# Optimization experiments

Measured on AMD Instinct MI355X. Metric: run time of the kernel, lower is better.

Reference implementation:

```python
import jax, jax.numpy as jnp
import numpy as np

N, L, LEADS = 512, 640, 3
COND_DIM, NUM_K, DIM_K = 1, 100, 5
FLAT = 256 * 79  # 20224, from conv stack trace


def _leaky(x):
    return jnp.where(x >= 0, x, 0.2 * x)


def _sn(w, u):
    # PyTorch spectral_norm: one power iteration (u, v detached), sigma = u^T W v
    wm = w.reshape(w.shape[0], -1)
    v = wm.T @ u
    v = v / (jnp.linalg.norm(v) + 1e-12)
    u2 = wm @ v
    u2 = u2 / (jnp.linalg.norm(u2) + 1e-12)
    u2 = jax.lax.stop_gradient(u2)
    v = jax.lax.stop_gradient(v)
    sigma = u2 @ (wm @ v)
    return w / sigma


def _conv1d(x, w, b, stride, pad):
    y = jax.lax.conv_general_dilated(
        x, w, window_strides=(stride,), padding=[(pad, pad)],
        dimension_numbers=('NCH', 'OIH', 'NCH'))
    return y + b[None, :, None]


def setup_inputs() -> dict:
    key = jax.random.key(0)
    ks = jax.random.split(key, 16)
    g = lambda k, shp, s: (jax.random.normal(k, shp, dtype=jnp.float32) * s)
    inp = {
        'ecg': jax.random.normal(ks[0], (N, L, LEADS), dtype=jnp.float32),
        'condition': jax.random.randint(ks[1], (N, 1), 0, 4),
        'w1': g(ks[2], (64, LEADS, 5), 0.2), 'b1': jnp.zeros((64,), jnp.float32),
        'u1': jax.random.normal(ks[3], (64,), dtype=jnp.float32),
        'w2': g(ks[4], (128, 64, 7), 0.05), 'b2': jnp.zeros((128,), jnp.float32),
        'u2': jax.random.normal(ks[5], (128,), dtype=jnp.float32),
        'w3': g(ks[6], (256, 128, 9), 0.03), 'b3': jnp.zeros((256,), jnp.float32),
        'u3': jax.random.normal(ks[7], (256,), dtype=jnp.float32),
        'emb': g(ks[8], (4, COND_DIM), 1.0),
        'cond_w': g(ks[9], (50, COND_DIM), 0.5), 'cond_b': jnp.zeros((50,), jnp.float32),
        'mb_w': g(ks[10], (FLAT, NUM_K * DIM_K), 0.01),
        'fc_w': g(ks[11], (1, FLAT + NUM_K + 50), 0.01), 'fc_b': jnp.zeros((1,), jnp.float32),
    }
    return inp


def reference(ecg, condition, w1, b1, u1, w2, b2, u2, w3, b3, u3,
              emb, cond_w, cond_b, mb_w, fc_w, fc_b):
    # condition embedding -> Linear(cond_dim, 50)
    cemb = emb[condition[:, 0]]                       # [N, cond_dim]
    cond = cemb @ cond_w.T + cond_b                   # [N, 50]

    x = ecg.transpose(0, 2, 1)                        # [N, 3, 640]
    x = _leaky(_conv1d(x, _sn(w1, u1), b1, 2, 4))     # [N, 64, 322]
    x = _leaky(_conv1d(x, _sn(w2, u2), b2, 2, 3))     # [N, 128, 161]
    x = _leaky(_conv1d(x, _sn(w3, u3), b3, 2, 2))     # [N, 256, 79]
    flat = x.reshape(x.shape[0], -1)                  # [N, 20224]

    # minibatch discrimination
    act = (flat @ mb_w).reshape(-1, NUM_K, DIM_K)     # [N, K, D]
    l1 = jnp.abs(act[:, None] - act[None, :]).sum(-1)  # [N, N, K]
    feats = jnp.exp(-l1).sum(axis=1)                  # [N, K]

    out = jnp.concatenate([flat, feats, cond], axis=1)
    return out @ fc_w.T + fc_b                        # [N, 1]
```

## Files before the change

kernel.cpp:

```cpp
#include <hip/hip_runtime.h>
#include <math.h>

#define NB 512
#define LIN 640
#define NLEADS 3
#define L1O 322
#define L2O 161
#define L3O 79
#define C1N 64
#define C2N 128
#define C3N 256
#define FLATSZ 20224
#define NUMK 100
#define DIMK 5
#define SPLITK 16

typedef __attribute__((ext_vector_type(8))) short short8;
typedef __attribute__((ext_vector_type(4))) float f32x4;

__device__ __forceinline__ unsigned short f2bf(float x){
  unsigned u = __builtin_bit_cast(unsigned, x);
  unsigned r = u + 0x7FFFu + ((u >> 16) & 1u);
  return (unsigned short)(r >> 16);
}
__device__ __forceinline__ float bf2f(unsigned short x){
  unsigned u = ((unsigned)x) << 16;
  return __builtin_bit_cast(float, u);
}

__device__ __forceinline__ float block_reduce_sum(float val, float* red){
#pragma unroll
  for(int off=32; off>0; off>>=1) val += __shfl_down(val, off, 64);
  int lane = threadIdx.x & 63;
  int wv = threadIdx.x >> 6;
  if(lane==0) red[wv] = val;
  __syncthreads();
  int nw = blockDim.x >> 6;
  float r = red[0];
  for(int i=1;i<nw;i++) r += red[i];
  __syncthreads();
  return r;
}

__global__ __launch_bounds__(256)
void sn_pass1(const float* __restrict__ w1, const float* __restrict__ u1,
              const float* __restrict__ w2, const float* __restrict__ u2,
              const float* __restrict__ w3, const float* __restrict__ u3,
              float* __restrict__ v_all, float* __restrict__ ss){
  __shared__ float red[4];
  int b = blockIdx.x, tid = threadIdx.x;
  const float* w; const float* u; int O, C, off, c, widx;
  if(b==0){ w=w1; u=u1; O=64;  C=15;   off=0;   c=tid;            widx=0; }
  else if(b<3){ w=w2; u=u2; O=128; C=448; off=16;  c=(b-1)*256+tid; widx=1; }
  else { w=w3; u=u3; O=256; C=1152; off=464; c=(b-3)*256+tid;      widx=2; }
  float vv = 0.f;
  if(c < C){
    for(int o=0;o<O;o+=4){
      vv += w[(o+0)*C+c]*u[o+0] + w[(o+1)*C+c]*u[o+1]
          + w[(o+2)*C+c]*u[o+2] + w[(o+3)*C+c]*u[o+3];
    }
    v_all[off + c] = vv;
  }
  float ps = (c < C) ? vv*vv : 0.f;
  float tot = block_reduce_sum(ps, red);
  if(tid==0) atomicAdd(&ss[widx], tot);
}

__global__ __launch_bounds__(256)
void sn_pass2(const float* __restrict__ w1, const float* __restrict__ w2,
              const float* __restrict__ w3, const float* __restrict__ v_all,
              float* __restrict__ Sun){
  int b = blockIdx.x, tid = threadIdx.x;
  int lane = tid & 63, wv = tid >> 6;
  const float* w; int C, off, o, widx;
  if(b < 16){ w=w1; C=15;   off=0;   o=b*4+wv;      widx=0; }
  else if(b < 48){ w=w2; C=448; off=16;  o=(b-16)*4+wv; widx=1; }
  else { w=w3; C=1152; off=464; o=(b-48)*4+wv;          widx=2; }
  float t = 0.f;
  for(int c=lane; c<C; c+=64) t += w[o*C+c]*v_all[off+c];
#pragma unroll
  for(int s=32; s>0; s>>=1) t += __shfl_down(t, s, 64);
  if(lane==0) atomicAdd(&Sun[widx], t*t);
}

__global__ void wprep_kernel(const float* __restrict__ w1, const float* __restrict__ w2,
                             const float* __restrict__ w3, const float* __restrict__ ss,
                             const float* __restrict__ Sun,
                             unsigned short* __restrict__ w1p, unsigned short* __restrict__ w2p,
                             unsigned short* __restrict__ w3p){
  float sc[3];
#pragma unroll
  for(int i=0;i<3;i++){
    float inv = 1.f/(sqrtf(ss[i])+1e-12f);
    float S = Sun[i]*inv*inv;
    sc[i] = (sqrtf(S)+1e-12f)/S;
  }
  int idx = blockIdx.x*256 + threadIdx.x;
  if(idx < C1N*32){
    int o = idx >> 5, kk = idx & 31;
    w1p[idx] = (kk < 15) ? f2bf(w1[o*15+kk]*sc[0]) : 0;
  }
  if(idx < C2N*448){
    int o = idx / 448, k2 = idx - o*448;
    int r = k2 >> 6, i = k2 & 63;
    w2p[idx] = f2bf(w2[o*448 + i*7 + r]*sc[1]);
  }
  if(idx < C3N*1152){
    int o = idx / 1152, k2 = idx - o*1152;
    int r = k2 >> 7, i = k2 & 127;
    w3p[idx] = f2bf(w3[o*1152 + i*9 + r]*sc[2]);
  }
}

__global__ __launch_bounds__(256, 2)
void conv123_mfma(const float* __restrict__ ecg, const unsigned short* __restrict__ w1p,
                  const float* __restrict__ b1, const unsigned short* __restrict__ w2p,
                  const float* __restrict__ b2, const unsigned short* __restrict__ w3p,
                  const float* __restrict__ b3, unsigned short* __restrict__ flatbf){
  __shared__ unsigned short y2buf[22712];
  __shared__ unsigned short slabs[13600];
  __shared__ unsigned short B1s[3328];
  int n = blockIdx.x, tid = threadIdx.x;
  int lane = tid & 63, w = tid >> 6;

  if(tid < 136){
    y2buf[tid] = 0;
    y2buf[82*136 + tid] = 0;
    y2buf[83*136 + tid] = 0;
    y2buf[11424 + tid] = 0;
    y2buf[11424 + 81*136 + tid] = 0;
    y2buf[11424 + 82*136 + tid] = 0;
  }

  const float* eb = ecg + (size_t)n*LIN*NLEADS;
  f32x4 zero4 = {0.f,0.f,0.f,0.f};

  for(int tile=0; tile<2; tile++){
    int c0    = tile ? 189 : 0;
    int tbase = tile ? 96  : 0;
    int suboff= tile ? -94 : 2;

    __syncthreads();
    {
      uint4 z = {0u,0u,0u,0u};
      uint4* zd = (uint4*)slabs;
#pragma unroll
      for(int q=0;q<7;q++){
        int f = q*256 + tid;
        if(f < 1700) zd[f] = z;
      }
    }
    if(tid < 208){
      int t1 = c0 + tid;
      int p0 = 2*t1 - 4;
      unsigned short row16[16];
      row16[15] = 0;
      if(p0 >= 0 && p0 <= 635){
        const float* f = eb + p0*NLEADS;
#pragma unroll
        for(int rp=0; rp<5; rp++)
#pragma unroll
          for(int i=0;i<3;i++)
            row16[i*5+rp] = f2bf(f[3*rp+i]);
      } else {
#pragma unroll
        for(int rp=0; rp<5; rp++){
          int p = p0 + rp;
          bool ok = (unsigned)p < (unsigned)LIN;
#pragma unroll
          for(int i=0;i<3;i++)
            row16[i*5+rp] = ok ? f2bf(eb[p*NLEADS+i]) : (unsigned short)0;
        }
      }
      unsigned* dst = (unsigned*)(B1s + tid*16);
#pragma unroll
      for(int q=0;q<8;q++)
        dst[q] = (unsigned)row16[2*q] | ((unsigned)row16[2*q+1] << 16);
    }
    __syncthreads();

    {
      short8 a1 = *(const short8*)(w1p + ((w*16 + (lane&15))<<5) + (lane>>4)*8);
      int cfrag = lane >> 4;
#pragma unroll
      for(int half=0; half<2; half++){
        int nt0 = half*7, ntc = half ? 6 : 7;
        f32x4 c1[7];
        for(int j=0;j<ntc;j++){
          int tp = (nt0+j)*16 + (lane&15);
          short8 b = {0,0,0,0,0,0,0,0};
          if(cfrag < 2) b = *(const short8*)(B1s + tp*16 + cfrag*8);
          c1[j] = __builtin_amdgcn_mfma_f32_16x16x32_bf16(a1, b, zero4, 0, 0, 0);
        }
#pragma unroll
        for(int reg=0;reg<4;reg++){
          int o = w*16 + (lane>>4)*4 + reg;
          float bias = b1[o];
          for(int j=0;j<ntc;j++){
            int tp = (nt0+j)*16 + (lane&15);
            int t1 = c0 + tp;
            int sub = (t1>>1) + suboff;
            if(t1 < L1O && sub < 100){
              float v = c1[j][reg] + bias;
              v = v>=0.f ? v : 0.2f*v;
              slabs[((t1&1)?6800:0) + sub*68 + o] = f2bf(v);
            }
          }
        }
      }
    }
    __syncthreads();

    f32x4 acc[2][6];
#pragma unroll
    for(int i=0;i<2;i++)
#pragma unroll
      for(int j=0;j<6;j++) acc[i][j] = zero4;

    const unsigned short* w2base = w2p + ((size_t)(w*2*16 + (lane&15)))*448 + (lane>>4)*8;
    short8 a_cur[2];
    a_cur[0] = *(const short8*)(w2base);
    a_cur[1] = *(const short8*)(w2base + 16*448);

    for(int ck=0; ck<14; ck++){
      short8 a_nxt[2];
      if(ck < 13){
        a_nxt[0] = *(const short8*)(w2base + (ck+1)*32);
        a_nxt[1] = *(const short8*)(w2base + 16*448 + (ck+1)*32);
      }
      int r = ck >> 1, i0 = (ck & 1)*32;
      int p = (r+1) & 1;
      int m = ((r-3) - p) >> 1;
      int base = (p?6800:0) + (m+2 + (lane&15))*68 + i0 + (lane>>4)*8;
      short8 b[6];
#pragma unroll
      for(int nt=0;nt<6;nt++)
        b[nt] = *(const short8*)(slabs + base + nt*16*68);
      __builtin_amdgcn_s_setprio(1);
#pragma unroll
      for(int mm=0;mm<2;mm++)
#pragma unroll
        for(int nt=0;nt<6;nt++)
          acc[mm][nt] = __builtin_amdgcn_mfma_f32_16x16x32_bf16(a_cur[mm], b[nt], acc[mm][nt], 0, 0, 0);
      __builtin_amdgcn_s_setprio(0);
      if(ck < 13){ a_cur[0] = a_nxt[0]; a_cur[1] = a_nxt[1]; }
    }

#pragma unroll
    for(int mm=0;mm<2;mm++){
#pragma unroll
      for(int reg=0;reg<4;reg++){
        int o = (w*2+mm)*16 + (lane>>4)*4 + reg;
        float bias = b2[o];
#pragma unroll
        for(int nt=0;nt<6;nt++){
          int tl = nt*16 + (lane&15);
          int t = tbase + tl;
          if(t < L2O){
            float v = acc[mm][nt][reg] + bias;
            v = v>=0.f ? v : 0.2f*v;
            y2buf[((t&1)?11424:0) + ((t>>1)+1)*136 + o] = f2bf(v);
          }
        }
      }
    }
  }
  __syncthreads();

  f32x4 acc3[4][5];
#pragma unroll
  for(int i=0;i<4;i++)
#pragma unroll
    for(int j=0;j<5;j++) acc3[i][j] = zero4;

  const unsigned short* wbase = w3p + ((size_t)(w*64) + (lane&15))*1152 + (lane>>4)*8;
  short8 abuf[3][4];
#pragma unroll
  for(int d=0; d<2; d++)
#pragma unroll
    for(int mm=0;mm<4;mm++)
      abuf[d][mm] = *(const short8*)(wbase + mm*16*1152 + d*32);

#pragma unroll
  for(int ck=0; ck<36; ck++){
    const int cur = ck % 3;
    const int nxt = (ck+2) % 3;
    if(ck+2 < 36){
      int kc = (ck+2)*32;
#pragma unroll
      for(int mm=0;mm<4;mm++)
        abuf[nxt][mm] = *(const short8*)(wbase + mm*16*1152 + kc);
    }
    int r = ck >> 2, i0 = (ck & 3) * 32;
    int cbase = ((r & 1) ? 11424 : 0) + (r >> 1)*136 + i0 + (lane>>4)*8;
    short8 b[5];
#pragma unroll
    for(int nt=0;nt<5;nt++){
      int t = nt*16 + (lane&15);
      b[nt] = *(const short8*)(y2buf + cbase + t*136);
    }
    __builtin_amdgcn_s_setprio(1);
#pragma unroll
    for(int mm=0;mm<4;mm++)
#pragma unroll
      for(int nt=0;nt<5;nt++)
        acc3[mm][nt] = __builtin_amdgcn_mfma_f32_16x16x32_bf16(abuf[cur][mm], b[nt], acc3[mm][nt], 0, 0, 0);
    __builtin_amdgcn_s_setprio(0);
  }
#pragma unroll
  for(int mm=0;mm<4;mm++){
#pragma unroll
    for(int reg=0;reg<4;reg++){
      int o = w*64 + mm*16 + (lane>>4)*4 + reg;
      float bias = b3[o];
#pragma unroll
      for(int nt=0;nt<5;nt++){
        int t = nt*16 + (lane&15);
        if(t < L3O){
          float v = acc3[mm][nt][reg] + bias;
          v = v>=0.f ? v : 0.2f*v;
          flatbf[(size_t)n*FLATSZ + o*L3O + t] = f2bf(v);
        }
      }
    }
  }
}

__global__ __launch_bounds__(256)
void mbw_transpose(const float* __restrict__ mbw, unsigned short* __restrict__ mbwT){
  __shared__ unsigned short tile[32][36];
  int k0 = blockIdx.x*32, n0 = blockIdx.y*32, tid = threadIdx.x;
  int r = tid >> 3, c4 = (tid & 7) * 4;
  int nbase = n0 + c4;
  if(nbase + 3 < 500){
    float4 v = *(const float4*)(mbw + (size_t)(k0+r)*500 + nbase);
    tile[r][c4+0] = f2bf(v.x);
    tile[r][c4+1] = f2bf(v.y);
    tile[r][c4+2] = f2bf(v.z);
    tile[r][c4+3] = f2bf(v.w);
  } else {
#pragma unroll
    for(int j=0;j<4;j++){
      int nn = nbase + j;
      float v = (nn < 500) ? mbw[(size_t)(k0+r)*500 + nn] : 0.f;
      tile[r][c4+j] = f2bf(v);
    }
  }
  __syncthreads();
  int nl = tid >> 3, kq = (tid & 7) * 4;
  unsigned short t0 = tile[kq+0][nl], t1 = tile[kq+1][nl];
  unsigned short t2 = tile[kq+2][nl], t3 = tile[kq+3][nl];
  uint2 p;
  p.x = (unsigned)t0 | ((unsigned)t1 << 16);
  p.y = (unsigned)t2 | ((unsigned)t3 << 16);
  *(uint2*)(mbwT + (size_t)(n0+nl)*FLATSZ + k0 + kq) = p;
}

__global__ __launch_bounds__(256, 4)
void mb_gemm_mfma(const unsigned short* __restrict__ flatbf, const unsigned short* __restrict__ mbwT,
                  float* __restrict__ part){
  __shared__ unsigned short As[2][4096];
  __shared__ unsigned short Bs[2][4096];
  int tid = threadIdx.x;
  int lane = tid & 63, w = tid >> 6;
  int m0 = blockIdx.x*64, n0 = blockIdx.y*64, bz = blockIdx.z;
  int s_start = bz*19 + (bz < 12 ? bz : 12);
  int s_count = 19 + (bz < 12 ? 1 : 0);

  int r0 = tid >> 3,        c80 = tid & 7;
  int r1 = 32 + (tid >> 3), c81 = tid & 7;
  const unsigned short* aptr0 = flatbf + (size_t)(m0+r0)*FLATSZ + c80*8;
  const unsigned short* aptr1 = flatbf + (size_t)(m0+r1)*FLATSZ + c81*8;
  const unsigned short* bptr0 = mbwT  + (size_t)(n0+r0)*FLATSZ + c80*8;
  const unsigned short* bptr1 = mbwT  + (size_t)(n0+r1)*FLATSZ + c81*8;
  int d0 = r0*64 + ((c80 ^ (r0 & 7)) * 8);
  int d1 = r1*64 + ((c81 ^ (r1 & 7)) * 8);

  f32x4 zero = {0.f,0.f,0.f,0.f};
  f32x4 acc[4];
#pragma unroll
  for(int i=0;i<4;i++) acc[i] = zero;

  int arow = w*16 + (lane&15);
  int af0 = arow*64 + ((((lane>>4)  ) ^ (arow & 7)) * 8);
  int af1 = arow*64 + (((4+(lane>>4)) ^ (arow & 7)) * 8);
  int bf0[4], bf1[4];
#pragma unroll
  for(int nt=0;nt<4;nt++){
    int br = nt*16 + (lane&15);
    bf0[nt] = br*64 + ((((lane>>4)  ) ^ (br & 7)) * 8);
    bf1[nt] = br*64 + (((4+(lane>>4)) ^ (br & 7)) * 8);
  }

  size_t koff = (size_t)s_start * 64;
  uint4 ra0 = *(const uint4*)(aptr0 + koff);
  uint4 ra1 = *(const uint4*)(aptr1 + koff);
  uint4 rb0 = *(const uint4*)(bptr0 + koff);
  uint4 rb1 = *(const uint4*)(bptr1 + koff);

  for(int s=0; s<s_count; s++){
    int cur = s & 1;
    *(uint4*)(As[cur] + d0) = ra0;
    *(uint4*)(As[cur] + d1) = ra1;
    *(uint4*)(Bs[cur] + d0) = rb0;
    *(uint4*)(Bs[cur] + d1) = rb1;
    koff += 64;
    if(s+1 < s_count){
      ra0 = *(const uint4*)(aptr0 + koff);
      ra1 = *(const uint4*)(aptr1 + koff);
      rb0 = *(const uint4*)(bptr0 + koff);
      rb1 = *(const uint4*)(bptr1 + koff);
    }
    __syncthreads();
    short8 a0 = *(const short8*)(As[cur] + af0);
    short8 a1 = *(const short8*)(As[cur] + af1);
    short8 b0h0 = *(const short8*)(Bs[cur] + bf0[0]);
    short8 b1h0 = *(const short8*)(Bs[cur] + bf0[1]);
    short8 b2h0 = *(const short8*)(Bs[cur] + bf0[2]);
    short8 b3h0 = *(const short8*)(Bs[cur] + bf0[3]);
    short8 b0h1 = *(const short8*)(Bs[cur] + bf1[0]);
    short8 b1h1 = *(const short8*)(Bs[cur] + bf1[1]);
    short8 b2h1 = *(const short8*)(Bs[cur] + bf1[2]);
    short8 b3h1 = *(const short8*)(Bs[cur] + bf1[3]);
    __builtin_amdgcn_s_setprio(1);
    acc[0] = __builtin_amdgcn_mfma_f32_16x16x32_bf16(a0, b0h0, acc[0], 0, 0, 0);
    acc[1] = __builtin_amdgcn_mfma_f32_16x16x32_bf16(a0, b1h0, acc[1], 0, 0, 0);
    acc[2] = __builtin_amdgcn_mfma_f32_16x16x32_bf16(a0, b2h0, acc[2], 0, 0, 0);
    acc[3] = __builtin_amdgcn_mfma_f32_16x16x32_bf16(a0, b3h0, acc[3], 0, 0, 0);
    acc[0] = __builtin_amdgcn_mfma_f32_16x16x32_bf16(a1, b0h1, acc[0], 0, 0, 0);
    acc[1] = __builtin_amdgcn_mfma_f32_16x16x32_bf16(a1, b1h1, acc[1], 0, 0, 0);
    acc[2] = __builtin_amdgcn_mfma_f32_16x16x32_bf16(a1, b2h1, acc[2], 0, 0, 0);
    acc[3] = __builtin_amdgcn_mfma_f32_16x16x32_bf16(a1, b3h1, acc[3], 0, 0, 0);
    __builtin_amdgcn_s_setprio(0);
  }
  float* po = part + (size_t)bz*NB*500;
#pragma unroll
  for(int nt=0;nt<4;nt++){
#pragma unroll
    for(int reg=0;reg<4;reg++){
      int m = m0 + w*16 + (lane>>4)*4 + reg;
      int c = n0 + nt*16 + (lane&15);
      if(c < 500) po[(size_t)m*500 + c] = acc[nt][reg];
    }
  }
}

__global__ void mb_reduce_kernel(const float* __restrict__ part, float* __restrict__ actT){
  int idx = blockIdx.x*256 + threadIdx.x;
  float s = 0.f;
#pragma unroll
  for(int z=0;z<SPLITK;z++) s += part[(size_t)z*NB*500 + idx];
  int n = idx/500, c = idx - n*500;
  actT[(size_t)c*NB + n] = s;
}

__global__ __launch_bounds__(256)
void feats_kernel(const float* __restrict__ actT, float* __restrict__ feats){
  __shared__ float ash[4][50];
  __shared__ float pred[4][4];
  int i0 = blockIdx.x*4, k0 = blockIdx.y*10;
  int tid = threadIdx.x, lane = tid & 63, wv = tid >> 6;
  if(tid < 200){
    int ii = tid/50, c = tid - ii*50;
    ash[ii][c] = actT[(size_t)(k0*5+c)*NB + i0 + ii];
  }
  __syncthreads();
  const float LOG2E = 1.4426950408889634f;
  int j1 = tid, j2 = tid + 256;
  for(int kk=0; kk<10; kk++){
    const float* r0 = actT + (size_t)(k0+kk)*5*NB;
    float xa0=r0[j1], xa1=r0[NB+j1], xa2=r0[2*NB+j1], xa3=r0[3*NB+j1], xa4=r0[4*NB+j1];
    float xb0=r0[j2], xb1=r0[NB+j2], xb2=r0[2*NB+j2], xb3=r0[3*NB+j2], xb4=r0[4*NB+j2];
    float f[4];
#pragma unroll
    for(int ii=0; ii<4; ii++){
      float a0=ash[ii][kk*5+0], a1=ash[ii][kk*5+1], a2=ash[ii][kk*5+2],
            a3=ash[ii][kk*5+3], a4=ash[ii][kk*5+4];
      float la = fabsf(xa0-a0)+fabsf(xa1-a1)+fabsf(xa2-a2)+fabsf(xa3-a3)+fabsf(xa4-a4);
      float lb = fabsf(xb0-a0)+fabsf(xb1-a1)+fabsf(xb2-a2)+fabsf(xb3-a3)+fabsf(xb4-a4);
      f[ii] = exp2f(-LOG2E*la) + exp2f(-LOG2E*lb);
    }
#pragma unroll
    for(int ii=0; ii<4; ii++){
      float v = f[ii];
#pragma unroll
      for(int s=32; s>0; s>>=1) v += __shfl_down(v, s, 64);
      if(lane==0) pred[wv][ii] = v;
    }
    __syncthreads();
    if(tid < 4){
      float v = pred[0][tid] + pred[1][tid] + pred[2][tid] + pred[3][tid];
      feats[(size_t)(i0+tid)*NUMK + k0 + kk] = v;
    }
    __syncthreads();
  }
}

__global__ void final_kernel(const unsigned short* __restrict__ flatbf, const float* __restrict__ feats,
                             const int* __restrict__ condition, const float* __restrict__ emb,
                             const float* __restrict__ cond_w, const float* __restrict__ cond_b,
                             const float* __restrict__ fc_w, const float* __restrict__ fc_b,
                             float* __restrict__ out){
  __shared__ float red[4];
  int n = blockIdx.x, tid = threadIdx.x;
  float s = 0.f;
  const unsigned short* fr = flatbf + (size_t)n*FLATSZ;
  for(int q=tid; q<FLATSZ/8; q+=256){
    uint4 u = *(const uint4*)(fr + q*8);
    float4 wa = *(const float4*)(fc_w + q*8);
    float4 wb = *(const float4*)(fc_w + q*8 + 4);
    s += bf2f((unsigned short)(u.x & 0xffff))*wa.x + bf2f((unsigned short)(u.x >> 16))*wa.y
       + bf2f((unsigned short)(u.y & 0xffff))*wa.z + bf2f((unsigned short)(u.y >> 16))*wa.w
       + bf2f((unsigned short)(u.z & 0xffff))*wb.x + bf2f((unsigned short)(u.z >> 16))*wb.y
       + bf2f((unsigned short)(u.w & 0xffff))*wb.z + bf2f((unsigned short)(u.w >> 16))*wb.w;
  }
  for(int k=tid;k<NUMK;k+=256) s += feats[n*NUMK+k]*fc_w[FLATSZ+k];
  float ce = emb[condition[n]];
  for(int j=tid;j<50;j+=256) s += (ce*cond_w[j]+cond_b[j])*fc_w[FLATSZ+NUMK+j];
  s = block_reduce_sum(s, red);
  if(tid==0) out[n] = s + fc_b[0];
}

extern "C" void kernel_launch(void* const* d_in, const int* in_sizes, int n_in,
                              void* d_out, int out_size, void* d_ws, size_t ws_size,
                              hipStream_t stream) {
  const float* ecg   = (const float*)d_in[0];
  const int*   cond  = (const int*)  d_in[1];
  const float* w1    = (const float*)d_in[2];
  const float* b1    = (const float*)d_in[3];
  const float* u1    = (const float*)d_in[4];
  const float* w2    = (const float*)d_in[5];
  const float* b2    = (const float*)d_in[6];
  const float* u2    = (const float*)d_in[7];
  const float* w3    = (const float*)d_in[8];
  const float* b3    = (const float*)d_in[9];
  const float* u3    = (const float*)d_in[10];
  const float* emb   = (const float*)d_in[11];
  const float* condw = (const float*)d_in[12];
  const float* condb = (const float*)d_in[13];
  const float* mbw   = (const float*)d_in[14];
  const float* fcw   = (const float*)d_in[15];
  const float* fcb   = (const float*)d_in[16];

  float* ws = (float*)d_ws;
  float* ssbuf = ws + 16;
  float* Sunbuf= ws + 24;
  float* v_all = ws + 32;
  unsigned short* w1p  = (unsigned short*)(ws + 1648);
  unsigned short* w2p  = (unsigned short*)(ws + 2672);
  unsigned short* w3p  = (unsigned short*)(ws + 31344);
  unsigned short* mbwT = (unsigned short*)(ws + 178800);
  float* part  = ws + 5454448;
  float* actT  = ws + 9550448;
  float* feats = ws + 9806448;
  unsigned short* flatbf = (unsigned short*)(ws + 9857648);

  hipMemsetAsync((char*)d_ws + 64, 0, 64, stream);
  sn_pass1<<<8, 256, 0, stream>>>(w1,u1,w2,u2,w3,u3, v_all, ssbuf);
  sn_pass2<<<112, 256, 0, stream>>>(w1,w2,w3, v_all, Sunbuf);
  wprep_kernel<<<1152, 256, 0, stream>>>(w1, w2, w3, ssbuf, Sunbuf, w1p, w2p, w3p);
  conv123_mfma<<<NB, 256, 0, stream>>>(ecg, w1p, b1, w2p, b2, w3p, b3, flatbf);
  mbw_transpose<<<dim3(632,16), 256, 0, stream>>>(mbw, mbwT);
  mb_gemm_mfma<<<dim3(8,8,SPLITK), 256, 0, stream>>>(flatbf, mbwT, part);
  mb_reduce_kernel<<<1000, 256, 0, stream>>>(part, actT);
  feats_kernel<<<dim3(128,10), 256, 0, stream>>>(actT, feats);
  final_kernel<<<NB, 256, 0, stream>>>(flatbf, feats, cond, emb, condw, condb, fcw, fcb, (float*)d_out);
}
```

Baseline: 292.4 us.

## Merge small kernels into two cooperative grid-synced persistent kernels

Replaces the spectral-norm passes, weight prep, mb_w transpose, reduce, feats and final kernels with two cooperative kernels of 1024 blocks that use grid.sync between phases. The mb_w transpose now runs alongside the first power-iteration step. The aim is to cut launch overhead and the memset while keeping the same work. In exchange it adds grid-wide barrier costs, and the grid-stride loops lose some parallelism in the phases that had many blocks. Sun_part aliases the part buffer, which is safe only because part is written later.

```diff
diff --git a/kernel.cpp b/kernel.cpp
--- a/kernel.cpp
+++ b/kernel.cpp
@@ -1,5 +1,8 @@
 #include <hip/hip_runtime.h>
+#include <hip/hip_cooperative_groups.h>
 #include <math.h>
+
+namespace cg = cooperative_groups;
 
 #define NB 512
 #define LIN 640
@@ -14,6 +17,7 @@
 #define NUMK 100
 #define DIMK 5
 #define SPLITK 16
+#define COOPG 1024
 
 typedef __attribute__((ext_vector_type(8))) short short8;
 typedef __attribute__((ext_vector_type(4))) float f32x4;
@@ -43,72 +47,118 @@
 }
 
 __global__ __launch_bounds__(256)
-void sn_pass1(const float* __restrict__ w1, const float* __restrict__ u1,
-              const float* __restrict__ w2, const float* __restrict__ u2,
-              const float* __restrict__ w3, const float* __restrict__ u3,
-              float* __restrict__ v_all, float* __restrict__ ss){
+void coop1_kernel(const float* __restrict__ w1, const float* __restrict__ u1,
+                  const float* __restrict__ w2, const float* __restrict__ u2,
+                  const float* __restrict__ w3, const float* __restrict__ u3,
+                  float* __restrict__ v_all, float* __restrict__ ss_part,
+                  float* __restrict__ Sun_part, const float* __restrict__ mbw,
+                  unsigned short* __restrict__ mbwT,
+                  unsigned short* __restrict__ w1p, unsigned short* __restrict__ w2p,
+                  unsigned short* __restrict__ w3p){
   __shared__ float red[4];
-  int b = blockIdx.x, tid = threadIdx.x;
-  const float* w; const float* u; int O, C, off, c, widx;
-  if(b==0){ w=w1; u=u1; O=64;  C=15;   off=0;   c=tid;            widx=0; }
-  else if(b<3){ w=w2; u=u2; O=128; C=448; off=16;  c=(b-1)*256+tid; widx=1; }
-  else { w=w3; u=u3; O=256; C=1152; off=464; c=(b-3)*256+tid;      widx=2; }
-  float vv = 0.f;
-  if(c < C){
-    for(int o=0;o<O;o+=4){
-      vv += w[(o+0)*C+c]*u[o+0] + w[(o+1)*C+c]*u[o+1]
-          + w[(o+2)*C+c]*u[o+2] + w[(o+3)*C+c]*u[o+3];
-    }
-    v_all[off + c] = vv;
-  }
-  float ps = (c < C) ? vv*vv : 0.f;
-  float tot = block_reduce_sum(ps, red);
-  if(tid==0) atomicAdd(&ss[widx], tot);
-}
-
-__global__ __launch_bounds__(256)
-void sn_pass2(const float* __restrict__ w1, const float* __restrict__ w2,
-              const float* __restrict__ w3, const float* __restrict__ v_all,
-              float* __restrict__ Sun){
-  int b = blockIdx.x, tid = threadIdx.x;
-  int lane = tid & 63, wv = tid >> 6;
-  const float* w; int C, off, o, widx;
-  if(b < 16){ w=w1; C=15;   off=0;   o=b*4+wv;      widx=0; }
-  else if(b < 48){ w=w2; C=448; off=16;  o=(b-16)*4+wv; widx=1; }
-  else { w=w3; C=1152; off=464; o=(b-48)*4+wv;          widx=2; }
-  float t = 0.f;
-  for(int c=lane; c<C; c+=64) t += w[o*C+c]*v_all[off+c];
-#pragma unroll
-  for(int s=32; s>0; s>>=1) t += __shfl_down(t, s, 64);
-  if(lane==0) atomicAdd(&Sun[widx], t*t);
-}
-
-__global__ void wprep_kernel(const float* __restrict__ w1, const float* __restrict__ w2,
-                             const float* __restrict__ w3, const float* __restrict__ ss,
-                             const float* __restrict__ Sun,
-                             unsigned short* __restrict__ w1p, unsigned short* __restrict__ w2p,
-                             unsigned short* __restrict__ w3p){
+  __shared__ unsigned short tile[32][36];
+  cg::grid_group grid = cg::this_grid();
+  int bid = blockIdx.x, tid = threadIdx.x;
+
+  if(bid < 8){
+    int b = bid;
+    const float* w; const float* u; int O, C, off, c;
+    if(b==0){ w=w1; u=u1; O=64;  C=15;   off=0;   c=tid; }
+    else if(b<3){ w=w2; u=u2; O=128; C=448; off=16;  c=(b-1)*256+tid; }
+    else { w=w3; u=u3; O=256; C=1152; off=464; c=(b-3)*256+tid; }
+    float vv = 0.f;
+    if(c < C){
+      for(int o=0;o<O;o+=4){
+        vv += w[(o+0)*C+c]*u[o+0] + w[(o+1)*C+c]*u[o+1]
+            + w[(o+2)*C+c]*u[o+2] + w[(o+3)*C+c]*u[o+3];
+      }
+      v_all[off + c] = vv;
+    }
+    float ps = (c < C) ? vv*vv : 0.f;
+    float tot = block_reduce_sum(ps, red);
+    if(tid==0) ss_part[b] = tot;
+  }
+
+  for(int tt = bid; tt < 632*16; tt += COOPG){
+    int k0 = (tt % 632)*32, n0 = (tt / 632)*32;
+    int r = tid >> 3, c4 = (tid & 7) * 4;
+    int nbase = n0 + c4;
+    if(nbase + 3 < 500){
+      float4 v = *(const float4*)(mbw + (size_t)(k0+r)*500 + nbase);
+      tile[r][c4+0] = f2bf(v.x);
+      tile[r][c4+1] = f2bf(v.y);
+      tile[r][c4+2] = f2bf(v.z);
+      tile[r][c4+3] = f2bf(v.w);
+    } else {
+#pragma unroll
+      for(int j=0;j<4;j++){
+        int nn = nbase + j;
+        float v = (nn < 500) ? mbw[(size_t)(k0+r)*500 + nn] : 0.f;
+        tile[r][c4+j] = f2bf(v);
+      }
+    }
+    __syncthreads();
+    int nl = tid >> 3, kq = (tid & 7) * 4;
+    unsigned short t0 = tile[kq+0][nl], t1 = tile[kq+1][nl];
+    unsigned short t2 = tile[kq+2][nl], t3 = tile[kq+3][nl];
+    uint2 p;
+    p.x = (unsigned)t0 | ((unsigned)t1 << 16);
+    p.y = (unsigned)t2 | ((unsigned)t3 << 16);
+    *(uint2*)(mbwT + (size_t)(n0+nl)*FLATSZ + k0 + kq) = p;
+    __syncthreads();
+  }
+
+  grid.sync();
+
+  if(bid < 112){
+    int b = bid;
+    int lane = tid & 63, wv = tid >> 6;
+    const float* w; int C, off, o;
+    if(b < 16){ w=w1; C=15;   off=0;   o=b*4+wv; }
+    else if(b < 48){ w=w2; C=448; off=16;  o=(b-16)*4+wv; }
+    else { w=w3; C=1152; off=464; o=(b-48)*4+wv; }
+    float t = 0.f;
+    for(int c=lane; c<C; c+=64) t += w[o*C+c]*v_all[off+c];
+#pragma unroll
+    for(int s=32; s>0; s>>=1) t += __shfl_down(t, s, 64);
+    if(lane==0) red[wv] = t*t;
+    __syncthreads();
+    if(tid==0) Sun_part[b] = red[0] + red[1] + red[2] + red[3];
+  }
+
+  grid.sync();
+
+  float ssv0 = ss_part[0];
+  float ssv1 = ss_part[1] + ss_part[2];
+  float ssv2 = ss_part[3] + ss_part[4] + ss_part[5] + ss_part[6] + ss_part[7];
+  float Sunv[3] = {0.f, 0.f, 0.f};
+  for(int b=0;b<112;b++){
+    int widx = (b<16) ? 0 : ((b<48) ? 1 : 2);
+    Sunv[widx] += Sun_part[b];
+  }
+  float ssv[3] = {ssv0, ssv1, ssv2};
   float sc[3];
 #pragma unroll
   for(int i=0;i<3;i++){
-    float inv = 1.f/(sqrtf(ss[i])+1e-12f);
-    float S = Sun[i]*inv*inv;
+    float inv = 1.f/(sqrtf(ssv[i])+1e-12f);
+    float S = Sunv[i]*inv*inv;
     sc[i] = (sqrtf(S)+1e-12f)/S;
   }
-  int idx = blockIdx.x*256 + threadIdx.x;
-  if(idx < C1N*32){
-    int o = idx >> 5, kk = idx & 31;
-    w1p[idx] = (kk < 15) ? f2bf(w1[o*15+kk]*sc[0]) : 0;
-  }
-  if(idx < C2N*448){
-    int o = idx / 448, k2 = idx - o*448;
-    int r = k2 >> 6, i = k2 & 63;
-    w2p[idx] = f2bf(w2[o*448 + i*7 + r]*sc[1]);
-  }
-  if(idx < C3N*1152){
-    int o = idx / 1152, k2 = idx - o*1152;
-    int r = k2 >> 7, i = k2 & 127;
-    w3p[idx] = f2bf(w3[o*1152 + i*9 + r]*sc[2]);
+  for(int idx = bid*256 + tid; idx < C3N*1152; idx += COOPG*256){
+    if(idx < C1N*32){
+      int o = idx >> 5, kk = idx & 31;
+      w1p[idx] = (kk < 15) ? f2bf(w1[o*15+kk]*sc[0]) : 0;
+    }
+    if(idx < C2N*448){
+      int o = idx / 448, k2 = idx - o*448;
+      int r = k2 >> 6, i = k2 & 63;
+      w2p[idx] = f2bf(w2[o*448 + i*7 + r]*sc[1]);
+    }
+    if(idx < C3N*1152){
+      int o = idx / 1152, k2 = idx - o*1152;
+      int r = k2 >> 7, i = k2 & 127;
+      w3p[idx] = f2bf(w3[o*1152 + i*9 + r]*sc[2]);
+    }
   }
 }
 
@@ -324,36 +374,6 @@
       }
     }
   }
-}
-
-__global__ __launch_bounds__(256)
-void mbw_transpose(const float* __restrict__ mbw, unsigned short* __restrict__ mbwT){
-  __shared__ unsigned short tile[32][36];
-  int k0 = blockIdx.x*32, n0 = blockIdx.y*32, tid = threadIdx.x;
-  int r = tid >> 3, c4 = (tid & 7) * 4;
-  int nbase = n0 + c4;
-  if(nbase + 3 < 500){
-    float4 v = *(const float4*)(mbw + (size_t)(k0+r)*500 + nbase);
-    tile[r][c4+0] = f2bf(v.x);
-    tile[r][c4+1] = f2bf(v.y);
-    tile[r][c4+2] = f2bf(v.z);
-    tile[r][c4+3] = f2bf(v.w);
-  } else {
-#pragma unroll
-    for(int j=0;j<4;j++){
-      int nn = nbase + j;
-      float v = (nn < 500) ? mbw[(size_t)(k0+r)*500 + nn] : 0.f;
-      tile[r][c4+j] = f2bf(v);
-    }
-  }
-  __syncthreads();
-  int nl = tid >> 3, kq = (tid & 7) * 4;
-  unsigned short t0 = tile[kq+0][nl], t1 = tile[kq+1][nl];
-  unsigned short t2 = tile[kq+2][nl], t3 = tile[kq+3][nl];
-  uint2 p;
-  p.x = (unsigned)t0 | ((unsigned)t1 << 16);
-  p.y = (unsigned)t2 | ((unsigned)t3 << 16);
-  *(uint2*)(mbwT + (size_t)(n0+nl)*FLATSZ + k0 + kq) = p;
 }
 
 __global__ __launch_bounds__(256, 4)
@@ -445,80 +465,88 @@
   }
 }
 
-__global__ void mb_reduce_kernel(const float* __restrict__ part, float* __restrict__ actT){
-  int idx = blockIdx.x*256 + threadIdx.x;
-  float s = 0.f;
-#pragma unroll
-  for(int z=0;z<SPLITK;z++) s += part[(size_t)z*NB*500 + idx];
-  int n = idx/500, c = idx - n*500;
-  actT[(size_t)c*NB + n] = s;
-}
-
 __global__ __launch_bounds__(256)
-void feats_kernel(const float* __restrict__ actT, float* __restrict__ feats){
+void coop2_kernel(const float* __restrict__ part, float* __restrict__ actT,
+                  float* __restrict__ feats,
+                  const unsigned short* __restrict__ flatbf, const int* __restrict__ condition,
+                  const float* __restrict__ emb, const float* __restrict__ cond_w,
+                  const float* __restrict__ cond_b, const float* __restrict__ fc_w,
+                  const float* __restrict__ fc_b, float* __restrict__ out){
   __shared__ float ash[4][50];
   __shared__ float pred[4][4];
-  int i0 = blockIdx.x*4, k0 = blockIdx.y*10;
-  int tid = threadIdx.x, lane = tid & 63, wv = tid >> 6;
-  if(tid < 200){
-    int ii = tid/50, c = tid - ii*50;
-    ash[ii][c] = actT[(size_t)(k0*5+c)*NB + i0 + ii];
-  }
-  __syncthreads();
+  __shared__ float red[4];
+  cg::grid_group grid = cg::this_grid();
+  int bid = blockIdx.x, tid = threadIdx.x;
+  int lane = tid & 63, wv = tid >> 6;
+
+  for(int idx = bid*256 + tid; idx < NB*500; idx += COOPG*256){
+    float s = 0.f;
+#pragma unroll
+    for(int z=0;z<SPLITK;z++) s += part[(size_t)z*NB*500 + idx];
+    int n = idx/500, c = idx - n*500;
+    actT[(size_t)c*NB + n] = s;
+  }
+
+  grid.sync();
+
   const float LOG2E = 1.4426950408889634f;
-  int j1 = tid, j2 = tid + 256;
-  for(int kk=0; kk<10; kk++){
-    const float* r0 = actT + (size_t)(k0+kk)*5*NB;
-    float xa0=r0[j1], xa1=r0[NB+j1], xa2=r0[2*NB+j1], xa3=r0[3*NB+j1], xa4=r0[4*NB+j1];
-    float xb0=r0[j2], xb1=r0[NB+j2], xb2=r0[2*NB+j2], xb3=r0[3*NB+j2], xb4=r0[4*NB+j2];
-    float f[4];
-#pragma unroll
-    for(int ii=0; ii<4; ii++){
-      float a0=ash[ii][kk*5+0], a1=ash[ii][kk*5+1], a2=ash[ii][kk*5+2],
-            a3=ash[ii][kk*5+3], a4=ash[ii][kk*5+4];
-      float la = fabsf(xa0-a0)+fabsf(xa1-a1)+fabsf(xa2-a2)+fabsf(xa3-a3)+fabsf(xa4-a4);
-      float lb = fabsf(xb0-a0)+fabsf(xb1-a1)+fabsf(xb2-a2)+fabsf(xb3-a3)+fabsf(xb4-a4);
-      f[ii] = exp2f(-LOG2E*la) + exp2f(-LOG2E*lb);
-    }
-#pragma unroll
-    for(int ii=0; ii<4; ii++){
-      float v = f[ii];
-#pragma unroll
-      for(int s=32; s>0; s>>=1) v += __shfl_down(v, s, 64);
-      if(lane==0) pred[wv][ii] = v;
-    }
-    __syncthreads();
-    if(tid < 4){
-      float v = pred[0][tid] + pred[1][tid] + pred[2][tid] + pred[3][tid];
-      feats[(size_t)(i0+tid)*NUMK + k0 + kk] = v;
-    }
-    __syncthreads();
-  }
-}
-
-__global__ void final_kernel(const unsigned short* __restrict__ flatbf, const float* __restrict__ feats,
-                             const int* __restrict__ condition, const float* __restrict__ emb,
-                             const float* __restrict__ cond_w, const float* __restrict__ cond_b,
-                             const float* __restrict__ fc_w, const float* __restrict__ fc_b,
-                             float* __restrict__ out){
-  __shared__ float red[4];
-  int n = blockIdx.x, tid = threadIdx.x;
-  float s = 0.f;
-  const unsigned short* fr = flatbf + (size_t)n*FLATSZ;
-  for(int q=tid; q<FLATSZ/8; q+=256){
-    uint4 u = *(const uint4*)(fr + q*8);
-    float4 wa = *(const float4*)(fc_w + q*8);
-    float4 wb = *(const float4*)(fc_w + q*8 + 4);
-    s += bf2f((unsigned short)(u.x & 0xffff))*wa.x + bf2f((unsigned short)(u.x >> 16))*wa.y
-       + bf2f((unsigned short)(u.y & 0xffff))*wa.z + bf2f((unsigned short)(u.y >> 16))*wa.w
-       + bf2f((unsigned short)(u.z & 0xffff))*wb.x + bf2f((unsigned short)(u.z >> 16))*wb.y
-       + bf2f((unsigned short)(u.w & 0xffff))*wb.z + bf2f((unsigned short)(u.w >> 16))*wb.w;
-  }
-  for(int k=tid;k<NUMK;k+=256) s += feats[n*NUMK+k]*fc_w[FLATSZ+k];
-  float ce = emb[condition[n]];
-  for(int j=tid;j<50;j+=256) s += (ce*cond_w[j]+cond_b[j])*fc_w[FLATSZ+NUMK+j];
-  s = block_reduce_sum(s, red);
-  if(tid==0) out[n] = s + fc_b[0];
+  for(int bw = bid; bw < 128*10; bw += COOPG){
+    int i0 = (bw & 127)*4, k0 = (bw >> 7)*10;
+    if(tid < 200){
+      int ii = tid/50, c = tid - ii*50;
+      ash[ii][c] = actT[(size_t)(k0*5+c)*NB + i0 + ii];
+    }
+    __syncthreads();
+    int j1 = tid, j2 = tid + 256;
+    for(int kk=0; kk<10; kk++){
+      const float* r0 = actT + (size_t)(k0+kk)*5*NB;
+      float xa0=r0[j1], xa1=r0[NB+j1], xa2=r0[2*NB+j1], xa3=r0[3*NB+j1], xa4=r0[4*NB+j1];
+      float xb0=r0[j2], xb1=r0[NB+j2], xb2=r0[2*NB+j2], xb3=r0[3*NB+j2], xb4=r0[4*NB+j2];
+      float f[4];
+#pragma unroll
+      for(int ii=0; ii<4; ii++){
+        float a0=ash[ii][kk*5+0], a1=ash[ii][kk*5+1], a2=ash[ii][kk*5+2],
+              a3=ash[ii][kk*5+3], a4=ash[ii][kk*5+4];
+        float la = fabsf(xa0-a0)+fabsf(xa1-a1)+fabsf(xa2-a2)+fabsf(xa3-a3)+fabsf(xa4-a4);
+        float lb = fabsf(xb0-a0)+fabsf(xb1-a1)+fabsf(xb2-a2)+fabsf(xb3-a3)+fabsf(xb4-a4);
+        f[ii] = exp2f(-LOG2E*la) + exp2f(-LOG2E*lb);
+      }
+#pragma unroll
+      for(int ii=0; ii<4; ii++){
+        float v = f[ii];
+#pragma unroll
+        for(int s=32; s>0; s>>=1) v += __shfl_down(v, s, 64);
+        if(lane==0) pred[wv][ii] = v;
+      }
+      __syncthreads();
+      if(tid < 4){
+        float v = pred[0][tid] + pred[1][tid] + pred[2][tid] + pred[3][tid];
+        feats[(size_t)(i0+tid)*NUMK + k0 + kk] = v;
+      }
+      __syncthreads();
+    }
+  }
+
+  grid.sync();
+
+  for(int n = bid; n < NB; n += COOPG){
+    float s = 0.f;
+    const unsigned short* fr = flatbf + (size_t)n*FLATSZ;
+    for(int q=tid; q<FLATSZ/8; q+=256){
+      uint4 u = *(const uint4*)(fr + q*8);
+      float4 wa = *(const float4*)(fc_w + q*8);
+      float4 wb = *(const float4*)(fc_w + q*8 + 4);
+      s += bf2f((unsigned short)(u.x & 0xffff))*wa.x + bf2f((unsigned short)(u.x >> 16))*wa.y
+         + bf2f((unsigned short)(u.y & 0xffff))*wa.z + bf2f((unsigned short)(u.y >> 16))*wa.w
+         + bf2f((unsigned short)(u.z & 0xffff))*wb.x + bf2f((unsigned short)(u.z >> 16))*wb.y
+         + bf2f((unsigned short)(u.w & 0xffff))*wb.z + bf2f((unsigned short)(u.w >> 16))*wb.w;
+    }
+    for(int k=tid;k<NUMK;k+=256) s += feats[n*NUMK+k]*fc_w[FLATSZ+k];
+    float ce = emb[condition[n]];
+    for(int j=tid;j<50;j+=256) s += (ce*cond_w[j]+cond_b[j])*fc_w[FLATSZ+NUMK+j];
+    s = block_reduce_sum(s, red);
+    if(tid==0) out[n] = s + fc_b[0];
+  }
 }
 
 extern "C" void kernel_launch(void* const* d_in, const int* in_sizes, int n_in,
@@ -543,26 +571,30 @@
   const float* fcb   = (const float*)d_in[16];
 
   float* ws = (float*)d_ws;
-  float* ssbuf = ws + 16;
-  float* Sunbuf= ws + 24;
-  float* v_all = ws + 32;
+  float* ss_part  = ws + 16;
+  float* v_all    = ws + 32;
   unsigned short* w1p  = (unsigned short*)(ws + 1648);
   unsigned short* w2p  = (unsigned short*)(ws + 2672);
   unsigned short* w3p  = (unsigned short*)(ws + 31344);
   unsigned short* mbwT = (unsigned short*)(ws + 178800);
   float* part  = ws + 5454448;
+  float* Sun_part = part;
   float* actT  = ws + 9550448;
   float* feats = ws + 9806448;
   unsigned short* flatbf = (unsigned short*)(ws + 9857648);
 
-  hipMemsetAsync((char*)d_ws + 64, 0, 64, stream);
-  sn_pass1<<<8, 256, 0, stream>>>(w1,u1,w2,u2,w3,u3, v_all, ssbuf);
-  sn_pass2<<<112, 256, 0, stream>>>(w1,w2,w3, v_all, Sunbuf);
-  wprep_kernel<<<1152, 256, 0, stream>>>(w1, w2, w3, ssbuf, Sunbuf, w1p, w2p, w3p);
+  {
+    void* a1[] = {(void*)&w1,(void*)&u1,(void*)&w2,(void*)&u2,(void*)&w3,(void*)&u3,
+                  (void*)&v_all,(void*)&ss_part,(void*)&Sun_part,(void*)&mbw,(void*)&mbwT,
+                  (void*)&w1p,(void*)&w2p,(void*)&w3p};
+    hipLaunchCooperativeKernel((const void*)coop1_kernel, dim3(COOPG), dim3(256), a1, 0, stream);
+  }
   conv123_mfma<<<NB, 256, 0, stream>>>(ecg, w1p, b1, w2p, b2, w3p, b3, flatbf);
-  mbw_transpose<<<dim3(632,16), 256, 0, stream>>>(mbw, mbwT);
   mb_gemm_mfma<<<dim3(8,8,SPLITK), 256, 0, stream>>>(flatbf, mbwT, part);
-  mb_reduce_kernel<<<1000, 256, 0, stream>>>(part, actT);
-  feats_kernel<<<dim3(128,10), 256, 0, stream>>>(actT, feats);
-  final_kernel<<<NB, 256, 0, stream>>>(flatbf, feats, cond, emb, condw, condb, fcw, fcb, (float*)d_out);
-}
+  {
+    void* a2[] = {(void*)&part,(void*)&actT,(void*)&feats,(void*)&flatbf,(void*)&cond,
+                  (void*)&emb,(void*)&condw,(void*)&condb,(void*)&fcw,(void*)&fcb,
+                  (void*)&d_out};
+    hipLaunchCooperativeKernel((const void*)coop2_kernel, dim3(COOPG), dim3(256), a2, 0, stream);
+  }
+}
```

Result: slower. 758.8 us (+159.5%).
